# Optimization experiments

Hardware: AMD Instinct MI355X
Metric: run time of the kernel (lower is better)

The kernel has to match this reference:

```python
import jax, jax.numpy as jnp
import numpy as np

# MaskingConfig constants
NUM_BLOCKS = 4          # config.num_target_blocks
SCALE_MIN = 0.15        # config.target_scale_min
SCALE_MAX = 0.2         # config.target_scale_max

BATCH = 256
SEQ_LEN = 131072


def setup_inputs() -> dict:
    key = jax.random.key(0)
    k1, k2 = jax.random.split(key)
    total_spans = BATCH * NUM_BLOCKS
    # uniform draws underlying torch's .uniform_() and torch.rand()
    scales_u = jax.random.uniform(k1, (total_spans,), dtype=jnp.float32)
    starts_u = jax.random.uniform(k2, (total_spans,), dtype=jnp.float32)
    return {"scales_u": scales_u, "starts_u": starts_u,
            "batch_size": BATCH, "seq_len": SEQ_LEN}


def reference(scales_u, starts_u, batch_size, seq_len):
    # scales ~ U(SCALE_MIN, SCALE_MAX)
    scales = SCALE_MIN + scales_u * (SCALE_MAX - SCALE_MIN)
    # span_lens = clamp(int(scales * seq_len), min=1); .int() truncates (positive -> floor)
    span_lens = jnp.maximum((scales * seq_len).astype(jnp.int32), 1)          # [T]
    max_starts = jnp.maximum(seq_len - span_lens, 0)                          # [T]
    # starts = int(rand * (max_starts + 1))
    starts = (starts_u * (max_starts.astype(jnp.float32) + 1.0)).astype(jnp.int32)
    ends = jnp.minimum(starts + span_lens, seq_len)                           # [T]

    pos = jnp.arange(seq_len, dtype=jnp.int32)                                # [S]
    # span coverage via broadcasted comparison: [T, S] bool
    cover = (pos[None, :] >= starts[:, None]) & (pos[None, :] < ends[:, None])
    # OR the num_blocks spans belonging to each batch item
    target_mask = cover.reshape(batch_size, NUM_BLOCKS, seq_len).any(axis=1)  # [B, S]
    context_mask = ~target_mask

    # padded replacement for the ragged per-batch nonzero list:
    # masked positions first (ascending), padded with seq_len sentinel
    padded_positions = jnp.sort(
        jnp.where(target_mask, pos[None, :], seq_len), axis=1)                # [B, S] int32
    return context_mask, target_mask, padded_positions
```

## Files before the change

kernel.cpp:

```cpp
#include <hip/hip_runtime.h>


constexpr int S_LEN = 131072;
constexpr int NBLK  = 4;
constexpr int TPB   = 256;
constexpr int ITEMS = 32;

typedef int int4v __attribute__((ext_vector_type(4)));

__global__ __launch_bounds__(TPB) void span_mask_kernel(
    const float* __restrict__ scales_u,
    const float* __restrict__ starts_u,
    int* __restrict__ out,
    int batch)
{
    const int b     = blockIdx.y;
    const int which = blockIdx.z;

    int ss[NBLK], ee[NBLK];
#pragma unroll
    for (int t = 0; t < NBLK; ++t) {
        float u  = scales_u[b * NBLK + t];
        float r  = starts_u[b * NBLK + t];
        float sc = __fadd_rn(0.15f, __fmul_rn(u, 0.05f));
        int len  = (int)__fmul_rn(sc, 131072.0f);
        if (len < 1) len = 1;
        int mx   = S_LEN - len; if (mx < 0) mx = 0;
        int st   = (int)__fmul_rn(r, __fadd_rn((float)mx, 1.0f));
        int en   = st + len; if (en > S_LEN) en = S_LEN;
        ss[t] = st; ee[t] = en;
    }

#define CSWAP(i, j)                                                        \
    if (ss[i] > ss[j]) {                                                   \
        int t0 = ss[i]; ss[i] = ss[j]; ss[j] = t0;                         \
        int t1 = ee[i]; ee[i] = ee[j]; ee[j] = t1;                         \
    }
    CSWAP(0, 1) CSWAP(2, 3) CSWAP(0, 2) CSWAP(1, 3) CSWAP(1, 2)
#undef CSWAP

    const int L0 = ss[0],          R0 = ee[0];
    const int L1 = max(ss[1], R0), R1 = max(ee[1], R0);
    const int L2 = max(ss[2], R1), R2 = max(ee[2], R1);
    const int L3 = max(ss[3], R2), R3 = max(ee[3], R2);
    const int c1 = R0 - L0;
    const int c2 = c1 + (R1 - L1);
    const int c3 = c2 + (R2 - L2);
    const int total = c3 + (R3 - L3);

    const size_t BS = (size_t)batch * S_LEN;
    int* __restrict__ dst = out + (size_t)which * BS + (size_t)b * S_LEN;

    const int blockStart = blockIdx.x * (TPB * ITEMS);

    if (which < 2) {
        const int flip = which ^ 1;
#pragma unroll
        for (int q = 0; q < ITEMS / 4; ++q) {
            const int s0 = blockStart + q * (TPB * 4) + threadIdx.x * 4;
            int v[4];
#pragma unroll
            for (int j = 0; j < 4; ++j) {
                const int s = s0 + j;
                const int cov =
                    ((s >= ss[0]) & (s < ee[0])) | ((s >= ss[1]) & (s < ee[1])) |
                    ((s >= ss[2]) & (s < ee[2])) | ((s >= ss[3]) & (s < ee[3]));
                v[j] = cov ^ flip;
            }
            int4v v4 = { v[0], v[1], v[2], v[3] };
            *(reinterpret_cast<int4v*>(dst + s0)) = v4;
        }
    } else {
#pragma unroll
        for (int q = 0; q < ITEMS / 4; ++q) {
            const int s0 = blockStart + q * (TPB * 4) + threadIdx.x * 4;
            int v[4];
#pragma unroll
            for (int j = 0; j < 4; ++j) {
                const int s = s0 + j;
                int p;
                if      (s >= total) p = S_LEN;
                else if (s >= c3)    p = L3 + (s - c3);
                else if (s >= c2)    p = L2 + (s - c2);
                else if (s >= c1)    p = L1 + (s - c1);
                else                 p = L0 + s;
                v[j] = p;
            }
            int4v v4 = { v[0], v[1], v[2], v[3] };
            *(reinterpret_cast<int4v*>(dst + s0)) = v4;
        }
    }
}

extern "C" void kernel_launch(void* const* d_in, const int* in_sizes, int n_in,
                              void* d_out, int out_size, void* d_ws, size_t ws_size,
                              hipStream_t stream)
{
    const float* scales_u = (const float*)d_in[0];
    const float* starts_u = (const float*)d_in[1];
    const int batch = 256;
    dim3 grid(S_LEN / (TPB * ITEMS), batch, 3);
    span_mask_kernel<<<grid, dim3(TPB), 0, stream>>>(
        scales_u, starts_u, (int*)d_out, batch);
}
```

Baseline: 79.54 us.

## Use persistent flat grid of 2048 blocks iterating over output chunks

Replaces the 3D grid of many small blocks (16x256x3) with a flat grid of 2048 blocks, each looping over a contiguous 48K-element slice of the whole output. Span parameters are recomputed only when the batch index changes within the loop. The goal is to cut block launch and scheduling overhead and keep each block's stores contiguous for this store-bound kernel. In exchange it adds per-iteration index math and a branch, and a rolled loop with less unrolling.

```diff
diff --git a/kernel.cpp b/kernel.cpp
--- a/kernel.cpp
+++ b/kernel.cpp
@@ -1,94 +1,101 @@
 #include <hip/hip_runtime.h>
 
 
-constexpr int S_LEN = 131072;
-constexpr int NBLK  = 4;
-constexpr int TPB   = 256;
-constexpr int ITEMS = 32;
+constexpr int S_LEN   = 131072;
+constexpr int BATCH   = 256;
+constexpr int TOTAL   = 3 * BATCH * S_LEN;
+constexpr int TPB     = 256;
+constexpr int NBLOCKS = 2048;
+constexpr int PER_BLK = TOTAL / NBLOCKS;
+constexpr int PER_IT  = TPB * 4;
+constexpr int NITER   = PER_BLK / PER_IT;
 
 typedef int int4v __attribute__((ext_vector_type(4)));
 
 __global__ __launch_bounds__(TPB) void span_mask_kernel(
     const float* __restrict__ scales_u,
     const float* __restrict__ starts_u,
-    int* __restrict__ out,
-    int batch)
+    int* __restrict__ out)
 {
-    const int b     = blockIdx.y;
-    const int which = blockIdx.z;
+    const int base = blockIdx.x * PER_BLK + threadIdx.x * 4;
 
-    int ss[NBLK], ee[NBLK];
+    int prev_b = -1;
+    int s0_ = 0, s1_ = 0, s2_ = 0, s3_ = 0;
+    int e0_ = 0, e1_ = 0, e2_ = 0, e3_ = 0;
+    int L0 = 0, L1 = 0, L2 = 0, L3 = 0;
+    int c1 = 0, c2 = 0, c3 = 0, total = 0;
+
+    for (int it = 0; it < NITER; ++it) {
+        const int flat  = base + it * PER_IT;
+        const int which = flat >> 25;
+        const int b     = (flat >> 17) & 255;
+        const int s     = flat & (S_LEN - 1);
+
+        if (b != prev_b) {
+            prev_b = b;
+            int ss[4], ee[4];
 #pragma unroll
-    for (int t = 0; t < NBLK; ++t) {
-        float u  = scales_u[b * NBLK + t];
-        float r  = starts_u[b * NBLK + t];
-        float sc = __fadd_rn(0.15f, __fmul_rn(u, 0.05f));
-        int len  = (int)__fmul_rn(sc, 131072.0f);
-        if (len < 1) len = 1;
-        int mx   = S_LEN - len; if (mx < 0) mx = 0;
-        int st   = (int)__fmul_rn(r, __fadd_rn((float)mx, 1.0f));
-        int en   = st + len; if (en > S_LEN) en = S_LEN;
-        ss[t] = st; ee[t] = en;
-    }
+            for (int t = 0; t < 4; ++t) {
+                float u  = scales_u[b * 4 + t];
+                float r  = starts_u[b * 4 + t];
+                float sc = __fadd_rn(0.15f, __fmul_rn(u, 0.05f));
+                int len  = (int)__fmul_rn(sc, 131072.0f);
+                if (len < 1) len = 1;
+                int mx   = S_LEN - len; if (mx < 0) mx = 0;
+                int st   = (int)__fmul_rn(r, __fadd_rn((float)mx, 1.0f));
+                int en   = st + len; if (en > S_LEN) en = S_LEN;
+                ss[t] = st; ee[t] = en;
+            }
+#define CSWAP(i, j)                                                        \
+            if (ss[i] > ss[j]) {                                           \
+                int t0 = ss[i]; ss[i] = ss[j]; ss[j] = t0;                 \
+                int t1 = ee[i]; ee[i] = ee[j]; ee[j] = t1;                 \
+            }
+            CSWAP(0, 1) CSWAP(2, 3) CSWAP(0, 2) CSWAP(1, 3) CSWAP(1, 2)
+#undef CSWAP
+            s0_ = ss[0]; s1_ = ss[1]; s2_ = ss[2]; s3_ = ss[3];
+            e0_ = ee[0]; e1_ = ee[1]; e2_ = ee[2]; e3_ = ee[3];
+            const int R0 = e0_;
+            L0 = s0_;
+            L1 = max(s1_, R0); const int R1 = max(e1_, R0);
+            L2 = max(s2_, R1); const int R2 = max(e2_, R1);
+            L3 = max(s3_, R2); const int R3 = max(e3_, R2);
+            c1 = R0 - L0;
+            c2 = c1 + (R1 - L1);
+            c3 = c2 + (R2 - L2);
+            total = c3 + (R3 - L3);
+        }
 
-#define CSWAP(i, j)                                                        \
-    if (ss[i] > ss[j]) {                                                   \
-        int t0 = ss[i]; ss[i] = ss[j]; ss[j] = t0;                         \
-        int t1 = ee[i]; ee[i] = ee[j]; ee[j] = t1;                         \
-    }
-    CSWAP(0, 1) CSWAP(2, 3) CSWAP(0, 2) CSWAP(1, 3) CSWAP(1, 2)
-#undef CSWAP
+        int v0, v1, v2, v3;
+        if (which == 2) {
+#define POSV(K, OUTV)                                                      \
+            {                                                              \
+                const int k = (K); int p;                                  \
+                if      (k >= total) p = S_LEN;                            \
+                else if (k >= c3)    p = L3 + (k - c3);                    \
+                else if (k >= c2)    p = L2 + (k - c2);                    \
+                else if (k >= c1)    p = L1 + (k - c1);                    \
+                else                 p = L0 + k;                           \
+                OUTV = p;                                                  \
+            }
+            POSV(s,     v0) POSV(s + 1, v1) POSV(s + 2, v2) POSV(s + 3, v3)
+#undef POSV
+        } else {
+            const int flip = which ^ 1;
+#define COVV(K, OUTV)                                                      \
+            {                                                              \
+                const int k = (K);                                         \
+                const int cov =                                            \
+                    ((k >= s0_) & (k < e0_)) | ((k >= s1_) & (k < e1_)) |  \
+                    ((k >= s2_) & (k < e2_)) | ((k >= s3_) & (k < e3_));   \
+                OUTV = cov ^ flip;                                         \
+            }
+            COVV(s,     v0) COVV(s + 1, v1) COVV(s + 2, v2) COVV(s + 3, v3)
+#undef COVV
+        }
 
-    const int L0 = ss[0],          R0 = ee[0];
-    const int L1 = max(ss[1], R0), R1 = max(ee[1], R0);
-    const int L2 = max(ss[2], R1), R2 = max(ee[2], R1);
-    const int L3 = max(ss[3], R2), R3 = max(ee[3], R2);
-    const int c1 = R0 - L0;
-    const int c2 = c1 + (R1 - L1);
-    const int c3 = c2 + (R2 - L2);
-    const int total = c3 + (R3 - L3);
-
-    const size_t BS = (size_t)batch * S_LEN;
-    int* __restrict__ dst = out + (size_t)which * BS + (size_t)b * S_LEN;
-
-    const int blockStart = blockIdx.x * (TPB * ITEMS);
-
-    if (which < 2) {
-        const int flip = which ^ 1;
-#pragma unroll
-        for (int q = 0; q < ITEMS / 4; ++q) {
-            const int s0 = blockStart + q * (TPB * 4) + threadIdx.x * 4;
-            int v[4];
-#pragma unroll
-            for (int j = 0; j < 4; ++j) {
-                const int s = s0 + j;
-                const int cov =
-                    ((s >= ss[0]) & (s < ee[0])) | ((s >= ss[1]) & (s < ee[1])) |
-                    ((s >= ss[2]) & (s < ee[2])) | ((s >= ss[3]) & (s < ee[3]));
-                v[j] = cov ^ flip;
-            }
-            int4v v4 = { v[0], v[1], v[2], v[3] };
-            *(reinterpret_cast<int4v*>(dst + s0)) = v4;
-        }
-    } else {
-#pragma unroll
-        for (int q = 0; q < ITEMS / 4; ++q) {
-            const int s0 = blockStart + q * (TPB * 4) + threadIdx.x * 4;
-            int v[4];
-#pragma unroll
-            for (int j = 0; j < 4; ++j) {
-                const int s = s0 + j;
-                int p;
-                if      (s >= total) p = S_LEN;
-                else if (s >= c3)    p = L3 + (s - c3);
-                else if (s >= c2)    p = L2 + (s - c2);
-                else if (s >= c1)    p = L1 + (s - c1);
-                else                 p = L0 + s;
-                v[j] = p;
-            }
-            int4v v4 = { v[0], v[1], v[2], v[3] };
-            *(reinterpret_cast<int4v*>(dst + s0)) = v4;
-        }
+        int4v v4 = { v0, v1, v2, v3 };
+        *(reinterpret_cast<int4v*>(out + flat)) = v4;
     }
 }
 
@@ -98,8 +105,6 @@
 {
     const float* scales_u = (const float*)d_in[0];
     const float* starts_u = (const float*)d_in[1];
-    const int batch = 256;
-    dim3 grid(S_LEN / (TPB * ITEMS), batch, 3);
-    span_mask_kernel<<<grid, dim3(TPB), 0, stream>>>(
-        scales_u, starts_u, (int*)d_out, batch);
+    span_mask_kernel<<<dim3(NBLOCKS), dim3(TPB), 0, stream>>>(
+        scales_u, starts_u, (int*)d_out);
 }
```

Result: slower. 86.05 us (+8.2%).
